# Optimization experiments

Hardware: AMD Instinct MI355X
Metric: run time of the kernel (lower is better)

## Reference

```python
import jax, jax.numpy as jnp
import numpy as np

NEG_SLOPE = 0.01  # torch leaky_relu default
EPS = 1e-12      # torch F.normalize default


def _edge_mlp(edge_attr, w1, b1, w2, b2, d_h):
    # Sequential(Linear, ReLU, Linear) -> per-edge weight matrices [E, d_h, d_h]
    h = jax.nn.relu(edge_attr @ w1 + b1)
    return (h @ w2 + b2).reshape(-1, d_h, d_h)


def _nnconv(h, src, dst, w_edge, root, bias, n_nodes):
    # message_j->i = x_j @ Theta(e_ji); aggregate (add) at dst; add root transform + bias
    msg = jnp.einsum('ei,eio->eo', h[src], w_edge)  # [E, d_h]
    agg = jax.ops.segment_sum(msg, dst, num_segments=n_nodes)
    return agg + h @ root + bias


def setup_inputs() -> dict:
    key = jax.random.key(0)
    ks = jax.random.split(key, 20)
    N, E, G = 20000, 200000, 128
    d_node, d_edge, d_h, d_out = 64, 16, 32, 32

    x = jax.random.normal(ks[0], (N, d_node), dtype=jnp.float32)
    edge_index = jax.random.randint(ks[1], (2, E), 0, N, dtype=jnp.int32)
    edge_attr = jax.random.normal(ks[2], (E, d_edge), dtype=jnp.float32)
    batch = jnp.sort(jax.random.randint(ks[3], (N,), 0, G, dtype=jnp.int32))

    def lin(k, fan_in, fan_out):
        kw, kb = jax.random.split(k)
        s = 1.0 / np.sqrt(fan_in)
        w = jax.random.uniform(kw, (fan_in, fan_out), jnp.float32, -s, s)
        b = jax.random.uniform(kb, (fan_out,), jnp.float32, -s, s)
        return w, b

    nfc_w, nfc_b = lin(ks[4], d_node, d_h)
    efc1_w1, efc1_b1 = lin(ks[5], d_edge, d_h)
    efc1_w2, efc1_b2 = lin(ks[6], d_h, d_h * d_h)
    root1 = jax.random.uniform(ks[7], (d_h, d_h), jnp.float32, -1/np.sqrt(d_h), 1/np.sqrt(d_h))
    bias1 = jnp.zeros((d_h,), jnp.float32)
    efc2_w1, efc2_b1 = lin(ks[8], d_edge, d_h)
    efc2_w2, efc2_b2 = lin(ks[9], d_h, d_h * d_h)
    root2 = jax.random.uniform(ks[10], (d_h, d_h), jnp.float32, -1/np.sqrt(d_h), 1/np.sqrt(d_h))
    bias2 = jnp.zeros((d_h,), jnp.float32)
    fc_w, fc_b = lin(ks[11], d_h, d_out)

    return dict(x=x, edge_index=edge_index, edge_attr=edge_attr, batch=batch,
                num_graphs=G,
                nfc_w=nfc_w, nfc_b=nfc_b,
                efc1_w1=efc1_w1, efc1_b1=efc1_b1, efc1_w2=efc1_w2, efc1_b2=efc1_b2,
                root1=root1, bias1=bias1,
                efc2_w1=efc2_w1, efc2_b1=efc2_b1, efc2_w2=efc2_w2, efc2_b2=efc2_b2,
                root2=root2, bias2=bias2,
                fc_w=fc_w, fc_b=fc_b)


def reference(x, edge_index, edge_attr, batch, num_graphs,
              nfc_w, nfc_b,
              efc1_w1, efc1_b1, efc1_w2, efc1_b2, root1, bias1,
              efc2_w1, efc2_b1, efc2_w2, efc2_b2, root2, bias2,
              fc_w, fc_b):
    n_nodes = x.shape[0]
    d_h = nfc_w.shape[1]
    src, dst = edge_index[0], edge_index[1]

    lrelu = lambda v: jax.nn.leaky_relu(v, NEG_SLOPE)
    # dropout(p=0.1) is identity at inference
    h = lrelu(x @ nfc_w + nfc_b)

    w_e1 = _edge_mlp(edge_attr, efc1_w1, efc1_b1, efc1_w2, efc1_b2, d_h)
    h = lrelu(_nnconv(h, src, dst, w_e1, root1, bias1, n_nodes))

    w_e2 = _edge_mlp(edge_attr, efc2_w1, efc2_b1, efc2_w2, efc2_b2, d_h)
    atom_embs = lrelu(_nnconv(h, src, dst, w_e2, root2, bias2, n_nodes))

    pooled = jax.ops.segment_sum(atom_embs, batch, num_segments=num_graphs)  # [G, d_h]
    norm = jnp.linalg.norm(pooled, ord=2, axis=1, keepdims=True)
    pooled = pooled / jnp.maximum(norm, EPS)

    out = pooled @ fc_w + fc_b
    return (out, atom_embs)
```

## Files before the change

### kernel.cpp

```cpp
#include <hip/hip_runtime.h>
#include <stdint.h>

#define NN 20000
#define NE 200000
#define NG 128
#define NJOBS 12500
#define SLOTS 2048

typedef __attribute__((ext_vector_type(8))) short short8;
typedef __attribute__((ext_vector_type(4))) float f32x4;
typedef __attribute__((ext_vector_type(4))) int   int4v;
typedef __attribute__((ext_vector_type(2))) unsigned int uint2v;

static __device__ __forceinline__ float bf2f(short s) {
    union { unsigned int u; float f; } x;
    x.u = ((unsigned int)(unsigned short)s) << 16;
    return x.f;
}
static __device__ __forceinline__ unsigned short f2bf(float f) {
    unsigned int u = __builtin_bit_cast(unsigned int, f);
    u += 0x7fffu + ((u >> 16) & 1u);
    return (unsigned short)(u >> 16);
}
static __device__ __forceinline__ unsigned int pack2bf(float a, float b) {
    unsigned int u0 = __builtin_bit_cast(unsigned int, a) + 0x8000u;
    unsigned int u1 = __builtin_bit_cast(unsigned int, b) + 0x8000u;
    return __builtin_amdgcn_perm(u1, u0, 0x07060302u);
}
static __device__ __forceinline__ int detect_isbf(const unsigned int* x) {
    unsigned int u = x[threadIdx.x & 63];
    unsigned int el = (u >> 7) & 0xffu;
    unsigned long long bm = __ballot((el >= 100u) && (el <= 140u));
    return __popcll(bm) > 32;
}

__global__ __launch_bounds__(256) void k_prep_all(
    const void* x, const void* nfcw, const void* nfcb,
    const void* root1, const void* bias1,
    const void* w2a, const void* b2a, const void* w2b, const void* b2b,
    const void* w1a, const void* b1a, const void* w1b, const void* b1b,
    const void* ea,
    float* __restrict__ h0, float* __restrict__ aggA, float* __restrict__ aggB,
    short* __restrict__ W2Ta, short* __restrict__ W2Tb,
    short* __restrict__ w1t_ws, float* __restrict__ b1f_ws,
    float* __restrict__ pooled, short* __restrict__ ea_ws) {
    const int isbf = detect_isbf((const unsigned int*)x);
    const int b = blockIdx.x;

    if (b < 2500) {
        __shared__ float wf[64 * 32];
        __shared__ float rf[32 * 32];
        __shared__ float bfs[32];
        __shared__ float rb[32];
        __shared__ float hrow[8][33];
        for (int i = threadIdx.x; i < 64 * 32; i += 256)
            wf[i] = isbf ? bf2f(((const short*)nfcw)[i]) : ((const float*)nfcw)[i];
        for (int i = threadIdx.x; i < 32 * 32; i += 256)
            rf[i] = isbf ? bf2f(((const short*)root1)[i]) : ((const float*)root1)[i];
        if (threadIdx.x < 32) {
            bfs[threadIdx.x] = isbf ? bf2f(((const short*)nfcb)[threadIdx.x])
                                    : ((const float*)nfcb)[threadIdx.x];
            rb[threadIdx.x]  = isbf ? bf2f(((const short*)bias1)[threadIdx.x])
                                    : ((const float*)bias1)[threadIdx.x];
        }
        __syncthreads();
        int t = b * 256 + threadIdx.x;
        int v = t >> 5, c = t & 31, vl = threadIdx.x >> 5;
        float acc = bfs[c];
        if (isbf) {
            const short* xr = (const short*)x + (size_t)v * 64;
#pragma unroll
            for (int q = 0; q < 64; ++q) acc += bf2f(xr[q]) * wf[q * 32 + c];
        } else {
            const float* xr = (const float*)x + (size_t)v * 64;
#pragma unroll
            for (int q = 0; q < 64; ++q) acc += xr[q] * wf[q * 32 + c];
        }
        float hv = acc > 0.f ? acc : 0.01f * acc;
        h0[t] = hv;
        hrow[vl][c] = hv;
        __syncthreads();
        float a2 = rb[c];
#pragma unroll
        for (int q = 0; q < 32; ++q) a2 += hrow[vl][q] * rf[q * 32 + c];
        aggA[t] = a2;
        return;
    }
    if (b < 4327) {
        const int bb = b - 2500;
        if (bb == 0) {
            for (int i = threadIdx.x; i < NG * 32; i += 256) pooled[i] = 0.f;
        }
        if (bb == 1) {
            for (int i = threadIdx.x; i < 1024; i += 256) {
                int layer = i >> 9, jj = i & 511, c = jj >> 4, q = jj & 15;
                const void* w1p = layer ? w1b : w1a;
                w1t_ws[i] = isbf ? ((const short*)w1p)[q * 32 + c]
                                 : (short)f2bf(((const float*)w1p)[q * 32 + c]);
            }
            for (int i = threadIdx.x; i < 64; i += 256) {
                int layer = i >> 5, c = i & 31;
                const void* b1p = layer ? b1b : b1a;
                b1f_ws[i] = isbf ? bf2f(((const short*)b1p)[c])
                                 : ((const float*)b1p)[c];
            }
        }
        int t = bb * 256 + threadIdx.x;
        if (t < 2 * 32 * 1056) {
            int layer = t / (32 * 1056);
            int r = t - layer * (32 * 1056);
            int o = r / 1056, kp = r - o * 1056;
            const void* w2 = layer ? w2b : w2a;
            const void* b2 = layer ? b2b : b2a;
            int idx; const void* sp;
            if (kp < 1024) { int kk = kp >> 5, i = kp & 31; idx = kk * 1024 + i * 32 + o; sp = w2; }
            else           { int i = kp - 1024;             idx = i * 32 + o;             sp = b2; }
            short v = isbf ? ((const short*)sp)[idx] : (short)f2bf(((const float*)sp)[idx]);
            (layer ? W2Tb : W2Ta)[o * 1056 + kp] = v;
            return;
        }
        int u = t - 2 * 32 * 1056;
        if (u < NE * 2 && !isbf) {
            const float* p = (const float*)ea + (size_t)u * 8;
            f32x4 f0 = *(const f32x4*)p;
            f32x4 f1 = *(const f32x4*)(p + 4);
            union { unsigned int d[4]; short8 v; } o8;
            o8.d[0] = pack2bf(f0[0], f0[1]);
            o8.d[1] = pack2bf(f0[2], f0[3]);
            o8.d[2] = pack2bf(f1[0], f1[1]);
            o8.d[3] = pack2bf(f1[2], f1[3]);
            *(short8*)&ea_ws[(size_t)u * 8] = o8.v;
        }
        return;
    }
    {
        int idx = (b - 4327) * 256 + threadIdx.x;
        if (idx < NN * 32 / 4) {
            f32x4 z = {0.f, 0.f, 0.f, 0.f};
            ((f32x4*)aggB)[idx] = z;
        }
    }
}

__global__ __launch_bounds__(256, 4) void k_edge(
    const float* __restrict__ h_in,
    const short* __restrict__ W2T,
    const short* __restrict__ w1pre,
    const float* __restrict__ b1pre,
    const int* __restrict__ src, const int* __restrict__ dst,
    const short* __restrict__ ea_bf,
    const short* __restrict__ ea_ws,
    const unsigned int* xdet,
    float* agg,
    const int layer2, const void* rootp, const void* biasp) {
    __shared__ __align__(16) short w2t[32 * 546];
    __shared__ __align__(16) short h1l[4 * 16 * 20];

    const int isbf = detect_isbf(xdet);
    const short* eap = isbf ? ea_bf : ea_ws;

    const int half = blockIdx.x & 1;
    const int k0   = half ? 512 : 0;
    const int S17  = half;
    const int KS   = 546;
    const int KLEN = half ? 544 : 512;

    {
        int cpr = KLEN >> 3;
        int chunks = 32 * cpr;
        for (int idx = threadIdx.x; idx < chunks; idx += 256) {
            int o = idx / cpr, t8 = idx - o * cpr;
            *(short8*)&w2t[o * KS + (t8 << 3)] =
                *(const short8*)&W2T[o * 1056 + k0 + (t8 << 3)];
        }
    }

    if (layer2) {
        const int base = blockIdx.x * 625;
        for (int i = threadIdx.x; i < 625; i += 256) {
            int t = base + i;
            int v = t >> 5, c = t & 31;
            const float* ar = h_in + (size_t)v * 32;
            float acc = isbf ? bf2f(((const short*)biasp)[c]) : ((const float*)biasp)[c];
#pragma unroll
            for (int q = 0; q < 32; ++q) {
                float hv = ar[q];
                hv = hv > 0.f ? hv : 0.01f * hv;
                float wv = isbf ? bf2f(((const short*)rootp)[q * 32 + c])
                                : ((const float*)rootp)[q * 32 + c];
                acc += hv * wv;
            }
            atomicAdd(&agg[t], acc);
        }
    }
    __syncthreads();

    const int lane = threadIdx.x & 63;
    const int wid  = threadIdx.x >> 6;
    const int m    = lane & 15;
    const int quad = lane >> 4;
    const int wb   = wid * (16 * 20);

    short8 w1frag = {0, 0, 0, 0, 0, 0, 0, 0};
    if (quad < 2) {
        int c = m + (half << 4);
        w1frag = *(const short8*)&w1pre[c * 16 + ((quad & 1) << 3)];
    }
    const float b1v = b1pre[m + (half << 4)];
    const f32x4 zero4 = {0.f, 0.f, 0.f, 0.f};

    int j = (blockIdx.x >> 1) * 4 + wid;

    short8 eafc;
    f32x4 hs[2];
    int srcn;
    int4v dvc;
    {
        const int e0 = j << 4;
        eafc = *(const short8*)&eap[(size_t)(e0 + m) * 16 + ((quad & 1) << 3)];
        int s0 = src[e0 + m];
        const float* hr = h_in + (size_t)s0 * 32 + (quad << 3);
        hs[0] = *(const f32x4*)hr;
        hs[1] = *(const f32x4*)(hr + 4);
        dvc = *(const int4v*)&dst[e0 + (quad << 2)];
        const int en = (j + SLOTS) < NJOBS ? ((j + SLOTS) << 4) : 0;
        srcn = src[en + m];
    }

    while (j < NJOBS) {
        const int jn = j + SLOTS;

        {
            f32x4 hacc = __builtin_amdgcn_mfma_f32_16x16x32_bf16(
                eafc, w1frag, zero4, 0, 0, 0);
            float v0 = fmaxf(hacc[0] + b1v, 0.f);
            float v1 = fmaxf(hacc[1] + b1v, 0.f);
            float v2 = fmaxf(hacc[2] + b1v, 0.f);
            float v3 = fmaxf(hacc[3] + b1v, 0.f);
            uint2v dl; dl[0] = pack2bf(v0, v1); dl[1] = pack2bf(v2, v3);
            *(uint2v*)&h1l[wb + m * 20 + (quad << 2)] = dl;
        }
        __asm volatile("s_waitcnt lgkmcnt(0)" ::: "memory");

        if (jn < NJOBS) {
            const int en = jn << 4;
            eafc = *(const short8*)&eap[(size_t)(en + m) * 16 + ((quad & 1) << 3)];
        }

        short8 hsbf;
        {
            f32x4 g0 = hs[0], g1 = hs[1];
            if (layer2) {
#pragma unroll
                for (int p = 0; p < 4; ++p) {
                    g0[p] = g0[p] > 0.f ? g0[p] : 0.01f * g0[p];
                    g1[p] = g1[p] > 0.f ? g1[p] : 0.01f * g1[p];
                }
            }
            union { unsigned int du[4]; short8 v; } a;
            a.du[0] = pack2bf(g0[0], g0[1]);
            a.du[1] = pack2bf(g0[2], g0[3]);
            a.du[2] = pack2bf(g1[0], g1[1]);
            a.du[3] = pack2bf(g1[2], g1[3]);
            hsbf = a.v;
        }

        int4v dvn = dvc;
        if (jn < NJOBS) {
            const float* hr = h_in + (size_t)srcn * 32 + (quad << 3);
            hs[0] = *(const f32x4*)hr;
            hs[1] = *(const f32x4*)(hr + 4);
            dvn = *(const int4v*)&dst[(jn << 4) + (quad << 2)];
            const int jn2 = jn + SLOTS;
            if (jn2 < NJOBS) srcn = src[(jn2 << 4) + m];
        }

        f32x4 acc0 = zero4, acc1 = zero4;
#pragma unroll
        for (int s = 0; s < 16; ++s) {
            short8 bf0 = *(const short8*)&w2t[m * KS + (s << 5) + (quad << 3)];
            short8 bf1 = *(const short8*)&w2t[(m + 16) * KS + (s << 5) + (quad << 3)];
            uint2v hd = *(const uint2v*)&h1l[wb + s * 20 + (quad << 2)];
            f32x4 hv;
            hv[0] = __builtin_bit_cast(float, hd[0] << 16);
            hv[1] = __builtin_bit_cast(float, hd[0] & 0xffff0000u);
            hv[2] = __builtin_bit_cast(float, hd[1] << 16);
            hv[3] = __builtin_bit_cast(float, hd[1] & 0xffff0000u);
            f32x4 u0 = __builtin_amdgcn_mfma_f32_16x16x32_bf16(hsbf, bf0, zero4, 0, 0, 0);
            f32x4 u1 = __builtin_amdgcn_mfma_f32_16x16x32_bf16(hsbf, bf1, zero4, 0, 0, 0);
            acc0 += hv * u0;
            acc1 += hv * u1;
        }
        if (S17) {
            const int s = 16;
            short8 bf0 = *(const short8*)&w2t[m * KS + (s << 5) + (quad << 3)];
            short8 bf1 = *(const short8*)&w2t[(m + 16) * KS + (s << 5) + (quad << 3)];
            acc0 = __builtin_amdgcn_mfma_f32_16x16x32_bf16(hsbf, bf0, acc0, 0, 0, 0);
            acc1 = __builtin_amdgcn_mfma_f32_16x16x32_bf16(hsbf, bf1, acc1, 0, 0, 0);
        }

#pragma unroll
        for (int r = 0; r < 4; ++r) {
            float* ap = agg + (size_t)dvc[r] * 32 + m;
            atomicAdd(ap, acc0[r]);
            atomicAdd(ap + 16, acc1[r]);
        }
        dvc = dvn;
        j = jn;
    }
}

__global__ __launch_bounds__(256) void k_final_nodes(
    const float* __restrict__ agg, const int* __restrict__ batch,
    const unsigned int* xdet, void* __restrict__ out, float* pooled) {
    const int isbf = detect_isbf(xdet);
    __shared__ float gacc[8][32];
    __shared__ int g0s;
    ((float*)gacc)[threadIdx.x] = 0.f;
    if (threadIdx.x == 0) g0s = batch[blockIdx.x * 8];
    __syncthreads();
    int t = blockIdx.x * 256 + threadIdx.x;
    float v = agg[t];
    v = v > 0.f ? v : 0.01f * v;
    if (isbf) ((short*)out)[4096 + t] = (short)f2bf(v);
    else      ((float*)out)[4096 + t] = v;
    int g = batch[t >> 5];
    int rel = g - g0s;
    int c = t & 31;
    if (rel < 8) atomicAdd(&gacc[rel][c], v);
    else         atomicAdd(&pooled[g * 32 + c], v);
    __syncthreads();
    {
        int gi = threadIdx.x >> 5, cc = threadIdx.x & 31;
        float s = gacc[gi][cc];
        if (s != 0.f) atomicAdd(&pooled[(g0s + gi) * 32 + cc], s);
    }
}

__global__ __launch_bounds__(64) void k_graph_out(
    const float* __restrict__ pooled, const void* fcw, const void* fcb,
    const unsigned int* xdet, void* __restrict__ out) {
    const int isbf = detect_isbf(xdet);
    int g = blockIdx.x;
    int t = threadIdx.x;
    __shared__ float pn[32];
    if (t < 32) {
        float p = pooled[g * 32 + t];
        float sq = p * p;
#pragma unroll
        for (int o = 16; o > 0; o >>= 1) sq += __shfl_xor(sq, o, 64);
        float inv = 1.0f / fmaxf(sqrtf(sq), 1e-12f);
        pn[t] = p * inv;
    }
    __syncthreads();
    if (t < 32) {
        float acc = isbf ? bf2f(((const short*)fcb)[t]) : ((const float*)fcb)[t];
#pragma unroll
        for (int q = 0; q < 32; ++q) {
            float wv = isbf ? bf2f(((const short*)fcw)[q * 32 + t])
                            : ((const float*)fcw)[q * 32 + t];
            acc += pn[q] * wv;
        }
        if (isbf) ((short*)out)[g * 32 + t] = (short)f2bf(acc);
        else      ((float*)out)[g * 32 + t] = acc;
    }
}

extern "C" void kernel_launch(void* const* d_in, const int* in_sizes, int n_in,
                              void* d_out, int out_size, void* d_ws, size_t ws_size,
                              hipStream_t stream) {
    (void)in_sizes; (void)n_in; (void)out_size; (void)ws_size;
    const void* x     = d_in[0];
    const int*  eidx  = (const int*)d_in[1];
    const void* ea    = d_in[2];
    const int*  batch = (const int*)d_in[3];
    const void* nfcw  = d_in[5];
    const void* nfcb  = d_in[6];
    const void* e1w1  = d_in[7];
    const void* e1b1  = d_in[8];
    const void* e1w2  = d_in[9];
    const void* e1b2  = d_in[10];
    const void* root1 = d_in[11];
    const void* bias1 = d_in[12];
    const void* e2w1  = d_in[13];
    const void* e2b1  = d_in[14];
    const void* e2w2  = d_in[15];
    const void* e2b2  = d_in[16];
    const void* root2 = d_in[17];
    const void* bias2 = d_in[18];
    const void* fcw   = d_in[19];
    const void* fcb   = d_in[20];
    const unsigned int* xdet = (const unsigned int*)x;

    char* ws = (char*)d_ws;
    float* h0     = (float*)ws; ws += (size_t)NN * 32 * 4;
    float* aggA   = (float*)ws; ws += (size_t)NN * 32 * 4;
    float* aggB   = (float*)ws; ws += (size_t)NN * 32 * 4;
    short* W2T1   = (short*)ws; ws += 32 * 1056 * 2;
    short* W2T2   = (short*)ws; ws += 32 * 1056 * 2;
    short* w1t_ws = (short*)ws; ws += 1024 * 2;
    float* b1f_ws = (float*)ws; ws += 64 * 4;
    float* pooled = (float*)ws; ws += NG * 32 * 4;
    short* ea_ws  = (short*)ws; ws += (size_t)NE * 16 * 2;

    const int* srcp = eidx;
    const int* dstp = eidx + NE;

    k_prep_all<<<4952, 256, 0, stream>>>(
        x, nfcw, nfcb, root1, bias1,
        e1w2, e1b2, e2w2, e2b2, e1w1, e1b1, e2w1, e2b1, ea,
        h0, aggA, aggB, W2T1, W2T2, w1t_ws, b1f_ws, pooled, ea_ws);

    k_edge<<<1024, 256, 0, stream>>>(h0, W2T1, w1t_ws, b1f_ws, srcp, dstp,
                                     (const short*)ea, ea_ws, xdet, aggA,
                                     0, nullptr, nullptr);
    k_edge<<<1024, 256, 0, stream>>>(aggA, W2T2, w1t_ws + 512, b1f_ws + 32, srcp, dstp,
                                     (const short*)ea, ea_ws, xdet, aggB,
                                     1, root2, bias2);
    k_final_nodes<<<(NN * 32 + 255) / 256, 256, 0, stream>>>(aggB, batch, xdet, d_out, pooled);
    k_graph_out<<<NG, 64, 0, stream>>>(pooled, fcw, fcb, xdet, d_out);
}
```

Before: 233.2 us.

## Restructure edge kernel to one-shot 32-edge jobs with full-K weights from global

```diff
diff --git a/kernel.cpp b/kernel.cpp
--- a/kernel.cpp
+++ b/kernel.cpp
@@ -4,8 +4,9 @@
 #define NN 20000
 #define NE 200000
 #define NG 128
-#define NJOBS 12500
-#define SLOTS 2048
+#define NJOBS 6250
+#define EGRID 1563
+#define L2SLICE 410
 
 typedef __attribute__((ext_vector_type(8))) short short8;
 typedef __attribute__((ext_vector_type(4))) float f32x4;
@@ -153,160 +154,148 @@
     const unsigned int* xdet,
     float* agg,
     const int layer2, const void* rootp, const void* biasp) {
-    __shared__ __align__(16) short w2t[32 * 546];
-    __shared__ __align__(16) short h1l[4 * 16 * 20];
+    __shared__ __align__(16) short h1l[4 * 32 * 36];
 
     const int isbf = detect_isbf(xdet);
     const short* eap = isbf ? ea_bf : ea_ws;
 
-    const int half = blockIdx.x & 1;
-    const int k0   = half ? 512 : 0;
-    const int S17  = half;
-    const int KS   = 546;
-    const int KLEN = half ? 544 : 512;
-
-    {
-        int cpr = KLEN >> 3;
-        int chunks = 32 * cpr;
-        for (int idx = threadIdx.x; idx < chunks; idx += 256) {
-            int o = idx / cpr, t8 = idx - o * cpr;
-            *(short8*)&w2t[o * KS + (t8 << 3)] =
-                *(const short8*)&W2T[o * 1056 + k0 + (t8 << 3)];
-        }
-    }
-
     if (layer2) {
-        const int base = blockIdx.x * 625;
-        for (int i = threadIdx.x; i < 625; i += 256) {
+        const int base = blockIdx.x * L2SLICE;
+        for (int i = threadIdx.x; i < L2SLICE; i += 256) {
             int t = base + i;
-            int v = t >> 5, c = t & 31;
-            const float* ar = h_in + (size_t)v * 32;
-            float acc = isbf ? bf2f(((const short*)biasp)[c]) : ((const float*)biasp)[c];
-#pragma unroll
-            for (int q = 0; q < 32; ++q) {
-                float hv = ar[q];
-                hv = hv > 0.f ? hv : 0.01f * hv;
-                float wv = isbf ? bf2f(((const short*)rootp)[q * 32 + c])
-                                : ((const float*)rootp)[q * 32 + c];
-                acc += hv * wv;
+            if (t < NN * 32) {
+                int v = t >> 5, c = t & 31;
+                const float* ar = h_in + (size_t)v * 32;
+                float acc = isbf ? bf2f(((const short*)biasp)[c]) : ((const float*)biasp)[c];
+#pragma unroll
+                for (int q = 0; q < 32; ++q) {
+                    float hv = ar[q];
+                    hv = hv > 0.f ? hv : 0.01f * hv;
+                    float wv = isbf ? bf2f(((const short*)rootp)[q * 32 + c])
+                                    : ((const float*)rootp)[q * 32 + c];
+                    acc += hv * wv;
+                }
+                atomicAdd(&agg[t], acc);
             }
-            atomicAdd(&agg[t], acc);
-        }
-    }
-    __syncthreads();
+        }
+    }
 
     const int lane = threadIdx.x & 63;
     const int wid  = threadIdx.x >> 6;
     const int m    = lane & 15;
     const int quad = lane >> 4;
-    const int wb   = wid * (16 * 20);
-
-    short8 w1frag = {0, 0, 0, 0, 0, 0, 0, 0};
+    const int wb   = wid * (32 * 36);
+
+    const int j = blockIdx.x * 4 + wid;
+    if (j >= NJOBS) return;
+
+    short8 w1lo = {0, 0, 0, 0, 0, 0, 0, 0};
+    short8 w1hi = {0, 0, 0, 0, 0, 0, 0, 0};
     if (quad < 2) {
-        int c = m + (half << 4);
-        w1frag = *(const short8*)&w1pre[c * 16 + ((quad & 1) << 3)];
-    }
-    const float b1v = b1pre[m + (half << 4)];
+        w1lo = *(const short8*)&w1pre[m * 16 + ((quad & 1) << 3)];
+        w1hi = *(const short8*)&w1pre[(m + 16) * 16 + ((quad & 1) << 3)];
+    }
+    const float b1lo = b1pre[m];
+    const float b1hi = b1pre[m + 16];
     const f32x4 zero4 = {0.f, 0.f, 0.f, 0.f};
 
-    int j = (blockIdx.x >> 1) * 4 + wid;
-
-    short8 eafc;
-    f32x4 hs[2];
-    int srcn;
-    int4v dvc;
+    const int e0 = j << 5;
+    short8 eafc[2];
+    f32x4 hs[2][2];
+    int4v dv[2];
     {
-        const int e0 = j << 4;
-        eafc = *(const short8*)&eap[(size_t)(e0 + m) * 16 + ((quad & 1) << 3)];
-        int s0 = src[e0 + m];
-        const float* hr = h_in + (size_t)s0 * 32 + (quad << 3);
-        hs[0] = *(const f32x4*)hr;
-        hs[1] = *(const f32x4*)(hr + 4);
-        dvc = *(const int4v*)&dst[e0 + (quad << 2)];
-        const int en = (j + SLOTS) < NJOBS ? ((j + SLOTS) << 4) : 0;
-        srcn = src[en + m];
-    }
-
-    while (j < NJOBS) {
-        const int jn = j + SLOTS;
-
-        {
-            f32x4 hacc = __builtin_amdgcn_mfma_f32_16x16x32_bf16(
-                eafc, w1frag, zero4, 0, 0, 0);
-            float v0 = fmaxf(hacc[0] + b1v, 0.f);
-            float v1 = fmaxf(hacc[1] + b1v, 0.f);
-            float v2 = fmaxf(hacc[2] + b1v, 0.f);
-            float v3 = fmaxf(hacc[3] + b1v, 0.f);
-            uint2v dl; dl[0] = pack2bf(v0, v1); dl[1] = pack2bf(v2, v3);
-            *(uint2v*)&h1l[wb + m * 20 + (quad << 2)] = dl;
-        }
-        __asm volatile("s_waitcnt lgkmcnt(0)" ::: "memory");
-
-        if (jn < NJOBS) {
-            const int en = jn << 4;
-            eafc = *(const short8*)&eap[(size_t)(en + m) * 16 + ((quad & 1) << 3)];
-        }
-
-        short8 hsbf;
-        {
-            f32x4 g0 = hs[0], g1 = hs[1];
-            if (layer2) {
-#pragma unroll
-                for (int p = 0; p < 4; ++p) {
-                    g0[p] = g0[p] > 0.f ? g0[p] : 0.01f * g0[p];
-                    g1[p] = g1[p] > 0.f ? g1[p] : 0.01f * g1[p];
-                }
+        int s0[2];
+#pragma unroll
+        for (int mt = 0; mt < 2; ++mt) {
+            eafc[mt] = *(const short8*)&eap[(size_t)(e0 + mt * 16 + m) * 16 + ((quad & 1) << 3)];
+            s0[mt] = src[e0 + mt * 16 + m];
+            dv[mt] = *(const int4v*)&dst[e0 + mt * 16 + (quad << 2)];
+        }
+#pragma unroll
+        for (int mt = 0; mt < 2; ++mt) {
+            const float* hr = h_in + (size_t)s0[mt] * 32 + (quad << 3);
+            hs[mt][0] = *(const f32x4*)hr;
+            hs[mt][1] = *(const f32x4*)(hr + 4);
+        }
+    }
+
+#pragma unroll
+    for (int mt = 0; mt < 2; ++mt) {
+        f32x4 alo = __builtin_amdgcn_mfma_f32_16x16x32_bf16(eafc[mt], w1lo, zero4, 0, 0, 0);
+        f32x4 ahi = __builtin_amdgcn_mfma_f32_16x16x32_bf16(eafc[mt], w1hi, zero4, 0, 0, 0);
+        float v0 = fmaxf(alo[0] + b1lo, 0.f);
+        float v1 = fmaxf(alo[1] + b1lo, 0.f);
+        float v2 = fmaxf(alo[2] + b1lo, 0.f);
+        float v3 = fmaxf(alo[3] + b1lo, 0.f);
+        uint2v dlo; dlo[0] = pack2bf(v0, v1); dlo[1] = pack2bf(v2, v3);
+        *(uint2v*)&h1l[wb + m * 36 + (mt << 4) + (quad << 2)] = dlo;
+        v0 = fmaxf(ahi[0] + b1hi, 0.f);
+        v1 = fmaxf(ahi[1] + b1hi, 0.f);
+        v2 = fmaxf(ahi[2] + b1hi, 0.f);
+        v3 = fmaxf(ahi[3] + b1hi, 0.f);
+        uint2v dhi; dhi[0] = pack2bf(v0, v1); dhi[1] = pack2bf(v2, v3);
+        *(uint2v*)&h1l[wb + (m + 16) * 36 + (mt << 4) + (quad << 2)] = dhi;
+    }
+    __asm volatile("s_waitcnt lgkmcnt(0)" ::: "memory");
+
+    short8 hsbf[2];
+#pragma unroll
+    for (int mt = 0; mt < 2; ++mt) {
+        f32x4 g0 = hs[mt][0], g1 = hs[mt][1];
+        if (layer2) {
+#pragma unroll
+            for (int p = 0; p < 4; ++p) {
+                g0[p] = g0[p] > 0.f ? g0[p] : 0.01f * g0[p];
+                g1[p] = g1[p] > 0.f ? g1[p] : 0.01f * g1[p];
             }
-            union { unsigned int du[4]; short8 v; } a;
-            a.du[0] = pack2bf(g0[0], g0[1]);
-            a.du[1] = pack2bf(g0[2], g0[3]);
-            a.du[2] = pack2bf(g1[0], g1[1]);
-            a.du[3] = pack2bf(g1[2], g1[3]);
-            hsbf = a.v;
-        }
-
-        int4v dvn = dvc;
-        if (jn < NJOBS) {
-            const float* hr = h_in + (size_t)srcn * 32 + (quad << 3);
-            hs[0] = *(const f32x4*)hr;
-            hs[1] = *(const f32x4*)(hr + 4);
-            dvn = *(const int4v*)&dst[(jn << 4) + (quad << 2)];
-            const int jn2 = jn + SLOTS;
-            if (jn2 < NJOBS) srcn = src[(jn2 << 4) + m];
-        }
-
-        f32x4 acc0 = zero4, acc1 = zero4;
-#pragma unroll
-        for (int s = 0; s < 16; ++s) {
-            short8 bf0 = *(const short8*)&w2t[m * KS + (s << 5) + (quad << 3)];
-            short8 bf1 = *(const short8*)&w2t[(m + 16) * KS + (s << 5) + (quad << 3)];
-            uint2v hd = *(const uint2v*)&h1l[wb + s * 20 + (quad << 2)];
+        }
+        union { unsigned int du[4]; short8 v; } a;
+        a.du[0] = pack2bf(g0[0], g0[1]);
+        a.du[1] = pack2bf(g0[2], g0[3]);
+        a.du[2] = pack2bf(g1[0], g1[1]);
+        a.du[3] = pack2bf(g1[2], g1[3]);
+        hsbf[mt] = a.v;
+    }
+
+    const short* wr0 = W2T + m * 1056 + (quad << 3);
+    const short* wr1 = W2T + (m + 16) * 1056 + (quad << 3);
+    f32x4 acc0[2] = {zero4, zero4}, acc1[2] = {zero4, zero4};
+#pragma unroll
+    for (int s = 0; s < 32; ++s) {
+        short8 bf0 = *(const short8*)(wr0 + (s << 5));
+        short8 bf1 = *(const short8*)(wr1 + (s << 5));
+#pragma unroll
+        for (int mt = 0; mt < 2; ++mt) {
+            uint2v hd = *(const uint2v*)&h1l[wb + s * 36 + (mt << 4) + (quad << 2)];
             f32x4 hv;
             hv[0] = __builtin_bit_cast(float, hd[0] << 16);
             hv[1] = __builtin_bit_cast(float, hd[0] & 0xffff0000u);
             hv[2] = __builtin_bit_cast(float, hd[1] << 16);
             hv[3] = __builtin_bit_cast(float, hd[1] & 0xffff0000u);
-            f32x4 u0 = __builtin_amdgcn_mfma_f32_16x16x32_bf16(hsbf, bf0, zero4, 0, 0, 0);
-            f32x4 u1 = __builtin_amdgcn_mfma_f32_16x16x32_bf16(hsbf, bf1, zero4, 0, 0, 0);
-            acc0 += hv * u0;
-            acc1 += hv * u1;
-        }
-        if (S17) {
-            const int s = 16;
-            short8 bf0 = *(const short8*)&w2t[m * KS + (s << 5) + (quad << 3)];
-            short8 bf1 = *(const short8*)&w2t[(m + 16) * KS + (s << 5) + (quad << 3)];
-            acc0 = __builtin_amdgcn_mfma_f32_16x16x32_bf16(hsbf, bf0, acc0, 0, 0, 0);
-            acc1 = __builtin_amdgcn_mfma_f32_16x16x32_bf16(hsbf, bf1, acc1, 0, 0, 0);
-        }
-
+            f32x4 u0 = __builtin_amdgcn_mfma_f32_16x16x32_bf16(hsbf[mt], bf0, zero4, 0, 0, 0);
+            f32x4 u1 = __builtin_amdgcn_mfma_f32_16x16x32_bf16(hsbf[mt], bf1, zero4, 0, 0, 0);
+            acc0[mt] += hv * u0;
+            acc1[mt] += hv * u1;
+        }
+    }
+    {
+        short8 bf0 = *(const short8*)(wr0 + 1024);
+        short8 bf1 = *(const short8*)(wr1 + 1024);
+#pragma unroll
+        for (int mt = 0; mt < 2; ++mt) {
+            acc0[mt] = __builtin_amdgcn_mfma_f32_16x16x32_bf16(hsbf[mt], bf0, acc0[mt], 0, 0, 0);
+            acc1[mt] = __builtin_amdgcn_mfma_f32_16x16x32_bf16(hsbf[mt], bf1, acc1[mt], 0, 0, 0);
+        }
+    }
+
+#pragma unroll
+    for (int mt = 0; mt < 2; ++mt) {
 #pragma unroll
         for (int r = 0; r < 4; ++r) {
-            float* ap = agg + (size_t)dvc[r] * 32 + m;
-            atomicAdd(ap, acc0[r]);
-            atomicAdd(ap + 16, acc1[r]);
-        }
-        dvc = dvn;
-        j = jn;
+            float* ap = agg + (size_t)dv[mt][r] * 32 + m;
+            atomicAdd(ap, acc0[mt][r]);
+            atomicAdd(ap + 16, acc1[mt][r]);
+        }
     }
 }
 
@@ -411,12 +400,12 @@
         e1w2, e1b2, e2w2, e2b2, e1w1, e1b1, e2w1, e2b1, ea,
         h0, aggA, aggB, W2T1, W2T2, w1t_ws, b1f_ws, pooled, ea_ws);
 
-    k_edge<<<1024, 256, 0, stream>>>(h0, W2T1, w1t_ws, b1f_ws, srcp, dstp,
-                                     (const short*)ea, ea_ws, xdet, aggA,
-                                     0, nullptr, nullptr);
-    k_edge<<<1024, 256, 0, stream>>>(aggA, W2T2, w1t_ws + 512, b1f_ws + 32, srcp, dstp,
-                                     (const short*)ea, ea_ws, xdet, aggB,
-                                     1, root2, bias2);
+    k_edge<<<EGRID, 256, 0, stream>>>(h0, W2T1, w1t_ws, b1f_ws, srcp, dstp,
+                                      (const short*)ea, ea_ws, xdet, aggA,
+                                      0, nullptr, nullptr);
+    k_edge<<<EGRID, 256, 0, stream>>>(aggA, W2T2, w1t_ws + 512, b1f_ws + 32, srcp, dstp,
+                                      (const short*)ea, ea_ws, xdet, aggB,
+                                      1, root2, bias2);
     k_final_nodes<<<(NN * 32 + 255) / 256, 256, 0, stream>>>(aggB, batch, xdet, d_out, pooled);
     k_graph_out<<<NG, 64, 0, stream>>>(pooled, fcw, fcb, xdet, d_out);
 }
```

Measured after the change: 232.9 us. No clear change (-0.1%).
